# Optimization experiments

Hardware: AMD Instinct MI355X
Metric: run time of the kernel (lower is better)

The kernel has to match this reference:

```python
import jax, jax.numpy as jnp
import numpy as np

D_MODEL = 1024
NUM_HEADS = 16
D_K = D_MODEL // NUM_HEADS
THETA = 10000.0
BATCH, SEQ = 2, 2048


def setup_inputs() -> dict:
    key = jax.random.key(0)
    k1, k2, k3 = jax.random.split(key, 3)
    x = jax.random.normal(k1, (BATCH, SEQ, D_MODEL), dtype=jnp.float32)
    token_positions = jnp.arange(SEQ, dtype=jnp.int64 if jax.config.jax_enable_x64 else jnp.int32)
    # torch.nn.Linear convention: weight [out_features, in_features], y = x @ W.T
    w_qkv = jax.random.normal(k2, (3 * D_MODEL, D_MODEL), dtype=jnp.float32) * 0.02
    w_o = jax.random.normal(k3, (D_MODEL, D_MODEL), dtype=jnp.float32) * 0.02
    return {"x": x, "token_positions": token_positions, "w_qkv": w_qkv, "w_o": w_o}


def _rope(v, positions):
    # v: [B, H, S, d_k]; positions: [S] int
    half = D_K // 2
    inv_freq = THETA ** (-jnp.arange(0, half, dtype=jnp.float32) / half)  # [half]
    angles = positions.astype(jnp.float32)[:, None] * inv_freq[None, :]   # [S, half]
    cos = jnp.cos(angles)  # [S, half]
    sin = jnp.sin(angles)
    v1 = v[..., 0::2]  # even dims [B,H,S,half]
    v2 = v[..., 1::2]  # odd dims
    r1 = v1 * cos - v2 * sin
    r2 = v1 * sin + v2 * cos
    # interleave back to [..., d_k]
    return jnp.stack([r1, r2], axis=-1).reshape(v.shape)


def reference(x, token_positions, w_qkv, w_o):
    B, S, _ = x.shape
    # fused QKV projection: [B,S,3*D] -> [B,S,3,H,d_k]
    qkv = jnp.einsum("bsd,ed->bse", x, w_qkv).reshape(B, S, 3, NUM_HEADS, D_K)
    q = jnp.transpose(qkv[:, :, 0], (0, 2, 1, 3))
    k = jnp.transpose(qkv[:, :, 1], (0, 2, 1, 3))
    v = jnp.transpose(qkv[:, :, 2], (0, 2, 1, 3))
    q = _rope(q, token_positions)
    k = _rope(k, token_positions)
    scale = 1.0 / jnp.sqrt(jnp.float32(D_K))
    scores = jnp.einsum("bhqd,bhkd->bhqk", q, k) * scale  # [B,H,S,S]
    causal = jnp.tril(jnp.ones((S, S), dtype=bool))
    scores = jnp.where(causal, scores, jnp.float32(-jnp.inf))
    attn = jax.nn.softmax(scores, axis=-1)
    out = jnp.einsum("bhqk,bhkd->bhqd", attn, v)  # [B,H,S,d_k]
    out = jnp.transpose(out, (0, 2, 1, 3)).reshape(B, S, D_MODEL)
    return jnp.einsum("bsd,ed->bse", out, w_o)
```

## Files before the change

### kernel.cpp

```cpp
#include <hip/hip_runtime.h>
#include <cstdint>
#include <cstddef>
#include <cmath>

#define D_MODEL 1024
#define NHEADS  16
#define DK      64
#define SEQ     2048
#define NBATCH  2

#define NEG_BIG (-1e30f)

typedef __attribute__((ext_vector_type(8))) short bf16x8;
typedef __attribute__((ext_vector_type(4))) short bf16x4;
typedef __attribute__((ext_vector_type(4))) float f32x4;

#if defined(__AMDGCN__)
#define SETPRIO(p) __builtin_amdgcn_s_setprio(p)
#else
#define SETPRIO(p)
#endif

__device__ __forceinline__ float fexp2(float x) {
#if defined(__AMDGCN__) && __has_builtin(__builtin_amdgcn_exp2f)
  return __builtin_amdgcn_exp2f(x);
#else
  return exp2f(x);
#endif
}

__device__ inline f32x4 mfma16x16x16(bf16x4 a, bf16x4 b, f32x4 c) {
#if defined(__AMDGCN__)
# if __has_builtin(__builtin_amdgcn_mfma_f32_16x16x16_bf16)
  return __builtin_amdgcn_mfma_f32_16x16x16_bf16(a, b, c, 0, 0, 0);
# else
  return __builtin_amdgcn_mfma_f32_16x16x16bf16_1k(a, b, c, 0, 0, 0);
# endif
#else
  (void)a; (void)b;
  return c;
#endif
}

__device__ inline void gll16(const unsigned short* g, unsigned short* l) {
#if defined(__AMDGCN__)
  __builtin_amdgcn_global_load_lds(
      (const __attribute__((address_space(1))) void*)g,
      (__attribute__((address_space(3))) void*)l, 16, 0, 0);
#else
  (void)g; (void)l;
#endif
}

__device__ inline unsigned short f2bf(float f) {
  unsigned int u = __float_as_uint(f);
  u += 0x7fffu + ((u >> 16) & 1u);
  return (unsigned short)(u >> 16);
}

__device__ __forceinline__ unsigned cvtpk_bf16(float lo, float hi) {
#if defined(__AMDGCN__)
  unsigned r;
  asm("v_cvt_pk_bf16_f32 %0, %1, %2" : "=v"(r) : "v"(lo), "v"(hi));
  return r;
#else
  return (unsigned)f2bf(lo) | ((unsigned)f2bf(hi) << 16);
#endif
}

__device__ __forceinline__ void cvt_block(const void* src,
                                          unsigned short* dst, int i0) {
  const unsigned short* sp =
      (const unsigned short*)src + (size_t)i0 * 8 + threadIdx.x * 8;
  int cnt = 0;
#pragma unroll
  for (int j = 0; j < 8; j += 2) {
    const unsigned int u = sp[j];
    cnt += (((u >> 7) & 0xFFu) >= 0x84u) ? 1 : 0;
  }
  __shared__ int red[256];
  red[threadIdx.x] = cnt;
  __syncthreads();
  for (int s = 128; s > 0; s >>= 1) {
    if (threadIdx.x < s) red[threadIdx.x] += red[threadIdx.x + s];
    __syncthreads();
  }
  const bool isf32 = red[0] > 64;

  const int i = i0 + threadIdx.x;
  if (isf32) {
    const float4* s = (const float4*)src;
    float4 a = s[2 * i], b = s[2 * i + 1];
    uint4 r;
    r.x = (unsigned)f2bf(a.x) | ((unsigned)f2bf(a.y) << 16);
    r.y = (unsigned)f2bf(a.z) | ((unsigned)f2bf(a.w) << 16);
    r.z = (unsigned)f2bf(b.x) | ((unsigned)f2bf(b.y) << 16);
    r.w = (unsigned)f2bf(b.z) | ((unsigned)f2bf(b.w) << 16);
    ((uint4*)dst)[i] = r;
  } else {
    ((uint4*)dst)[i] = ((const uint4*)src)[i];
  }
}

__global__ __launch_bounds__(256) void cvt2_kernel(
    const void* __restrict__ srcA, unsigned short* __restrict__ dstA, int n8A,
    const void* __restrict__ srcB, unsigned short* __restrict__ dstB, int n8B) {
  const int bi = blockIdx.x;
  const int nblkA = n8A >> 8;
  (void)n8B;
  if (bi < nblkA) cvt_block(srcA, dstA, bi << 8);
  else            cvt_block(srcB, dstB, (bi - nblkA) << 8);
}

__global__ __launch_bounds__(256) void cvt3_kernel(
    const void* __restrict__ srcA, unsigned short* __restrict__ dstA, int n8A,
    const void* __restrict__ srcB, unsigned short* __restrict__ dstB, int n8B,
    const void* __restrict__ srcC, unsigned short* __restrict__ dstC) {
  const int bi = blockIdx.x;
  const int nblkA = n8A >> 8;
  const int nblkB = n8B >> 8;
  if (bi < nblkA)               cvt_block(srcA, dstA, bi << 8);
  else if (bi < nblkA + nblkB)  cvt_block(srcB, dstB, (bi - nblkA) << 8);
  else                          cvt_block(srcC, dstC, (bi - nblkA - nblkB) << 8);
}

template <int NF>
__device__ inline void gemm_bt_t(const unsigned short* __restrict__ A,
                                 const unsigned short* __restrict__ W,
                                 int m0, int n0,
                                 unsigned short* As, unsigned short* Bs,
                                 f32x4 (&acc)[NF][4]) {
  const int t    = threadIdx.x;
  const int lane = t & 63;
  const int w    = t >> 6;
  const int wm   = (w >> 1) * 64;
  const int wn   = (w & 1) * (NF * 16);
  const int frow = lane & 15;
  const int q4   = lane >> 4;

  for (int ft = 0; ft < NF; ++ft)
    for (int tt = 0; tt < 4; ++tt)
      acc[ft][tt] = (f32x4){0.f, 0.f, 0.f, 0.f};

  const int srow  = t >> 3;
  const int gslot = t & 7;

  for (int k0 = 0; k0 < 1024; k0 += 64) {
    __syncthreads();
#pragma unroll
    for (int c = 0; c < 4; ++c) {
      const int row = c * 32 + srow;
      const int gsrc = gslot ^ (row & 7);
      gll16(A + (size_t)(m0 + row) * 1024 + k0 + gsrc * 8,
            As + ((size_t)t + 256 * c) * 8);
    }
#pragma unroll
    for (int c = 0; c < NF; ++c) {
      const int row = c * 32 + srow;
      const int gsrc = gslot ^ (row & 7);
      gll16(W + (size_t)(n0 + row) * 1024 + k0 + gsrc * 8,
            Bs + ((size_t)t + 256 * c) * 8);
    }
    __syncthreads();

#pragma unroll
    for (int kk = 0; kk < 2; ++kk) {
      const int gg = q4 + kk * 4;
      bf16x8 xv[4], wv[NF];
#pragma unroll
      for (int tt = 0; tt < 4; ++tt) {
        const int row = wm + tt * 16 + frow;
        xv[tt] = *(const bf16x8*)(As + row * 64 + ((gg ^ (row & 7)) << 3));
      }
#pragma unroll
      for (int ft = 0; ft < NF; ++ft) {
        const int row = wn + ft * 16 + frow;
        wv[ft] = *(const bf16x8*)(Bs + row * 64 + ((gg ^ (row & 7)) << 3));
      }
#pragma unroll
      for (int ft = 0; ft < NF; ++ft)
#pragma unroll
        for (int tt = 0; tt < 4; ++tt)
          acc[ft][tt] = __builtin_amdgcn_mfma_f32_16x16x32_bf16(wv[ft], xv[tt],
                                                                acc[ft][tt], 0, 0, 0);
    }
  }
}

__global__ __launch_bounds__(256) void qkv_rope_kernel(
    const unsigned short* __restrict__ x,
    const unsigned short* __restrict__ wqkv,
    unsigned short* __restrict__ Qw, unsigned short* __restrict__ Kw,
    unsigned short* __restrict__ Vw) {
  __shared__ __align__(16) unsigned short As[128 * 64];
  __shared__ __align__(16) unsigned short Bs[128 * 64];
  f32x4 acc[4][4];
  const int lin = blockIdx.y * 32 + blockIdx.x;
  const int c8  = lin & 7;
  const int i   = lin >> 3;
  const int m0  = (c8 * 4 + (i & 3)) * 128;
  const int n0  = (i >> 2) * 128;
  gemm_bt_t<4>(x, wqkv, m0, n0, As, Bs, acc);

  const int t = threadIdx.x, lane = t & 63, w = t >> 6;
  const int wm = (w >> 1) * 64, wn = (w & 1) * 64;
  const int i16 = lane & 15, q4 = lane >> 4;
  const int part = n0 >> 10;
  const float LN_THETA_OVER_HALF = 0.2878231366242558f;
  const float SCALE_L2E = 0.18033688011112042f;

#pragma unroll
  for (int ft = 0; ft < 4; ++ft) {
    const int nb0 = n0 + wn + ft * 16 + (q4 << 2);
    const int h  = (nb0 >> 6) & 15;
    const int d0 = nb0 & 63;
    const float invf0 = __expf(-(float)(d0 >> 1) * LN_THETA_OVER_HALF);
    const float invf1 = __expf(-(float)((d0 >> 1) + 1) * LN_THETA_OVER_HALF);
#pragma unroll
    for (int tt = 0; tt < 4; ++tt) {
      const int m = m0 + wm + tt * 16 + i16;
      const int b = m >> 11, s = m & 2047;
      float v0 = acc[ft][tt][0], v1 = acc[ft][tt][1];
      float v2 = acc[ft][tt][2], v3 = acc[ft][tt][3];
      if (part < 2) {
        float sn0, cs0, sn1, cs1;
        __sincosf((float)s * invf0, &sn0, &cs0);
        __sincosf((float)s * invf1, &sn1, &cs1);
        const float r0 = v0 * cs0 - v1 * sn0;
        const float r1 = v0 * sn0 + v1 * cs0;
        const float r2 = v2 * cs1 - v3 * sn1;
        const float r3 = v2 * sn1 + v3 * cs1;
        v0 = r0; v1 = r1; v2 = r2; v3 = r3;
        if (part == 0) {
          v0 *= SCALE_L2E; v1 *= SCALE_L2E; v2 *= SCALE_L2E; v3 *= SCALE_L2E;
        }
        ushort4 pk;
        pk.x = f2bf(v0); pk.y = f2bf(v1); pk.z = f2bf(v2); pk.w = f2bf(v3);
        unsigned short* dst = (part == 0) ? Qw : Kw;
        *(ushort4*)(dst + (((size_t)(b * NHEADS + h)) * SEQ + s) * DK + d0) = pk;
      } else {
        unsigned short* vt =
            Vw + (((size_t)(b * NHEADS + h)) * DK + d0) * SEQ + s;
        vt[0]       = f2bf(v0);
        vt[SEQ]     = f2bf(v1);
        vt[2 * SEQ] = f2bf(v2);
        vt[3 * SEQ] = f2bf(v3);
      }
    }
  }
}

__device__ __forceinline__ void softmax_upd(
    const f32x4 (&s)[2][4], int q4,
    float& m_i, float& l_i, f32x4 o[4], bf16x4 (&pf)[2][4]) {
  float tm = NEG_BIG;
#pragma unroll
  for (int u = 0; u < 2; ++u)
#pragma unroll
    for (int mt = 0; mt < 4; ++mt)
#pragma unroll
      for (int r = 0; r < 4; ++r) tm = fmaxf(tm, s[u][mt][r]);
  tm = fmaxf(tm, __shfl_xor(tm, 16, 64));
  tm = fmaxf(tm, __shfl_xor(tm, 32, 64));
  const float m_new = fmaxf(m_i, tm);
  const float alpha = fexp2(m_i - m_new);
  m_i = m_new;

  float ls = 0.f;
#pragma unroll
  for (int u = 0; u < 2; ++u)
#pragma unroll
    for (int mt = 0; mt < 4; ++mt) {
      float p0 = fexp2(s[u][mt][0] - m_new);
      float p1 = fexp2(s[u][mt][1] - m_new);
      float p2 = fexp2(s[u][mt][2] - m_new);
      float p3 = fexp2(s[u][mt][3] - m_new);
      ls += (p0 + p1) + (p2 + p3);
      union { unsigned uu[2]; bf16x4 v; } pkk;
      pkk.uu[0] = cvtpk_bf16(p0, p1);
      pkk.uu[1] = cvtpk_bf16(p2, p3);
      pf[u][mt] = pkk.v;
    }
  ls += __shfl_xor(ls, 16, 64);
  ls += __shfl_xor(ls, 32, 64);
  l_i = l_i * alpha + ls;

  float a4[4];
#pragma unroll
  for (int r = 0; r < 4; ++r) a4[r] = __shfl(alpha, (q4 << 2) + r, 64);
#pragma unroll
  for (int n = 0; n < 4; ++n)
#pragma unroll
    for (int r = 0; r < 4; ++r) o[n][r] *= a4[r];
}

__device__ __forceinline__ void attn_step(
    const unsigned short* Ks0, const unsigned short* Ks1,
    const unsigned short* Vt0, const unsigned short* Vt1,
    bf16x8 qf0, bf16x8 qf1, int i16, int q4, int w,
    int q0t, int kt2, bool domask,
    float& m_i, float& l_i, f32x4 o_acc[4]) {
  f32x4 s_acc[2][4];
  SETPRIO(1);
#pragma unroll
  for (int u = 0; u < 2; ++u) {
    const unsigned short* Ksu = u ? Ks1 : Ks0;
#pragma unroll
    for (int mt = 0; mt < 4; ++mt) {
      const int key = mt * 16 + i16;
      const int k7 = key & 7;
      bf16x8 a0 = *(const bf16x8*)(Ksu + key * 64 + ((q4 ^ k7) << 3));
      bf16x8 a1 = *(const bf16x8*)(Ksu + key * 64 + (((4 + q4) ^ k7) << 3));
      f32x4 acc = (f32x4){0.f, 0.f, 0.f, 0.f};
      acc = __builtin_amdgcn_mfma_f32_16x16x32_bf16(a0, qf0, acc, 0, 0, 0);
      acc = __builtin_amdgcn_mfma_f32_16x16x32_bf16(a1, qf1, acc, 0, 0, 0);
      s_acc[u][mt] = acc;
    }
  }
  SETPRIO(0);

  if (domask) {
    const int qrow = q0t + w * 16 + i16;
#pragma unroll
    for (int u = 0; u < 2; ++u) {
      const int kb2 = (kt2 + u) * 64 + q4 * 4;
#pragma unroll
      for (int mt = 0; mt < 4; ++mt)
#pragma unroll
        for (int r = 0; r < 4; ++r)
          if (kb2 + mt * 16 + r > qrow) s_acc[u][mt][r] = NEG_BIG;
    }
  }

  bf16x4 pf[2][4];
  softmax_upd(s_acc, q4, m_i, l_i, o_acc, pf);

  SETPRIO(1);
#pragma unroll
  for (int u = 0; u < 2; ++u) {
    const unsigned short* Vtu = u ? Vt1 : Vt0;
#pragma unroll
    for (int mt = 0; mt < 4; ++mt) {
#pragma unroll
      for (int nt = 0; nt < 4; ++nt) {
        const int dk = nt * 16 + i16;
        const int slot = ((mt << 1) | (q4 >> 1)) ^ (dk & 7);
        bf16x4 vb = *(const bf16x4*)(Vtu + dk * 64 + (slot << 3) + ((q4 & 1) << 2));
        o_acc[nt] = mfma16x16x16(pf[u][mt], vb, o_acc[nt]);
      }
    }
  }
  SETPRIO(0);
}

__device__ __forceinline__ void attn_step2(
    const unsigned short* Ks0, const unsigned short* Ks1,
    const unsigned short* Vt0, const unsigned short* Vt1,
    bf16x8 qfB0, bf16x8 qfB1, bf16x8 qfA0, bf16x8 qfA1,
    int i16, int q4, int w, int q0A, int kt2, bool domaskA,
    float& mB, float& lB, f32x4 oB[4],
    float& mA, float& lA, f32x4 oA[4]) {
  f32x4 sB[2][4], sA[2][4];
  SETPRIO(1);
#pragma unroll
  for (int u = 0; u < 2; ++u) {
    const unsigned short* Ksu = u ? Ks1 : Ks0;
#pragma unroll
    for (int mt = 0; mt < 4; ++mt) {
      const int key = mt * 16 + i16;
      const int k7 = key & 7;
      bf16x8 a0 = *(const bf16x8*)(Ksu + key * 64 + ((q4 ^ k7) << 3));
      bf16x8 a1 = *(const bf16x8*)(Ksu + key * 64 + (((4 + q4) ^ k7) << 3));
      f32x4 ab = (f32x4){0.f, 0.f, 0.f, 0.f};
      ab = __builtin_amdgcn_mfma_f32_16x16x32_bf16(a0, qfB0, ab, 0, 0, 0);
      ab = __builtin_amdgcn_mfma_f32_16x16x32_bf16(a1, qfB1, ab, 0, 0, 0);
      sB[u][mt] = ab;
      f32x4 aa = (f32x4){0.f, 0.f, 0.f, 0.f};
      aa = __builtin_amdgcn_mfma_f32_16x16x32_bf16(a0, qfA0, aa, 0, 0, 0);
      aa = __builtin_amdgcn_mfma_f32_16x16x32_bf16(a1, qfA1, aa, 0, 0, 0);
      sA[u][mt] = aa;
    }
  }
  SETPRIO(0);

  if (domaskA) {
    const int qrow = q0A + w * 16 + i16;
#pragma unroll
    for (int u = 0; u < 2; ++u) {
      const int kb2 = (kt2 + u) * 64 + q4 * 4;
#pragma unroll
      for (int mt = 0; mt < 4; ++mt)
#pragma unroll
        for (int r = 0; r < 4; ++r)
          if (kb2 + mt * 16 + r > qrow) sA[u][mt][r] = NEG_BIG;
    }
  }

  bf16x4 pfB[2][4], pfA[2][4];
  softmax_upd(sB, q4, mB, lB, oB, pfB);
  softmax_upd(sA, q4, mA, lA, oA, pfA);

  SETPRIO(1);
#pragma unroll
  for (int u = 0; u < 2; ++u) {
    const unsigned short* Vtu = u ? Vt1 : Vt0;
#pragma unroll
    for (int mt = 0; mt < 4; ++mt) {
#pragma unroll
      for (int nt = 0; nt < 4; ++nt) {
        const int dk = nt * 16 + i16;
        const int slot = ((mt << 1) | (q4 >> 1)) ^ (dk & 7);
        bf16x4 vb = *(const bf16x4*)(Vtu + dk * 64 + (slot << 3) + ((q4 & 1) << 2));
        oB[nt] = mfma16x16x16(pfB[u][mt], vb, oB[nt]);
        oA[nt] = mfma16x16x16(pfA[u][mt], vb, oA[nt]);
      }
    }
  }
  SETPRIO(0);
}

__global__ __launch_bounds__(256, 2) void attn_mfma_kernel(
    const unsigned short* __restrict__ Q, const unsigned short* __restrict__ K,
    const unsigned short* __restrict__ VT, unsigned short* __restrict__ O) {
  __shared__ __align__(16) unsigned short Ks[2][2][64 * 64];
  __shared__ __align__(16) unsigned short Vt[2][2][64 * 64];

  const int t = threadIdx.x, w = t >> 6, lane = t & 63;
  const int i16 = lane & 15, q4 = lane >> 4;
  const int lin = blockIdx.y * 16 + blockIdx.x;
  const int c8  = lin & 7;
  const int j   = lin >> 3;
  const int bh  = c8 * 4 + (j & 3);
  const int qbA = j >> 2;
  const int qbB = 31 - qbA;
  const int q0A = qbA * 64, q0B = qbB * 64;
  const size_t base = (size_t)bh * SEQ * DK;

  const int srow  = t >> 3;
  const int gslot = t & 7;

  auto stage = [&](int p, int buf) {
#pragma unroll
    for (int c = 0; c < 4; ++c) {
      const int row = srow + 32 * c;
      const int gs  = gslot ^ (row & 7);
      gll16(K + base + (size_t)(p * 128 + row) * DK + gs * 8,
            &Ks[buf][0][0] + ((size_t)t + 256 * c) * 8);
    }
#pragma unroll
    for (int c = 0; c < 4; ++c) {
      const int row = srow + 32 * c;
      const int gs  = gslot ^ (row & 7);
      gll16(VT + base + (size_t)(row & 63) * SEQ
               + p * 128 + (row >> 6) * 64 + gs * 8,
            &Vt[buf][0][0] + ((size_t)t + 256 * c) * 8);
    }
  };

  bf16x8 qfA0, qfA1, qfB0, qfB1;
  {
    const unsigned short* qpA = Q + base + (size_t)(q0A + w * 16 + i16) * DK + q4 * 8;
    qfA0 = *(const bf16x8*)(qpA);
    qfA1 = *(const bf16x8*)(qpA + 32);
    const unsigned short* qpB = Q + base + (size_t)(q0B + w * 16 + i16) * DK + q4 * 8;
    qfB0 = *(const bf16x8*)(qpB);
    qfB1 = *(const bf16x8*)(qpB + 32);
  }

  f32x4 oA[4], oB[4];
#pragma unroll
  for (int n = 0; n < 4; ++n) {
    oA[n] = (f32x4){0.f, 0.f, 0.f, 0.f};
    oB[n] = (f32x4){0.f, 0.f, 0.f, 0.f};
  }
  float mA = NEG_BIG, lA = 0.f, mB = NEG_BIG, lB = 0.f;

  const int npairA = (qbA >> 1) + 1;
  const int npairB = (qbB >> 1) + 1;

  stage(0, 0);

  for (int pr = 0; pr < npairB; ++pr) {
    const int kt2 = pr * 2;
    const int cb = pr & 1;
    __syncthreads();
    if (pr + 1 < npairB) stage(pr + 1, cb ^ 1);

    if (pr < npairA) {
      attn_step2(Ks[cb][0], Ks[cb][1], Vt[cb][0], Vt[cb][1],
                 qfB0, qfB1, qfA0, qfA1, i16, q4, w,
                 q0A, kt2, pr == npairA - 1,
                 mB, lB, oB, mA, lA, oA);
    } else {
      attn_step(Ks[cb][0], Ks[cb][1], Vt[cb][0], Vt[cb][1], qfB0, qfB1,
                i16, q4, w, q0B, kt2, pr == npairB - 1, mB, lB, oB);
    }
  }

  const int b = bh >> 4, h = bh & 15;
#pragma unroll
  for (int r = 0; r < 4; ++r) {
    const float lrA = __shfl(lA, (q4 << 2) + r, 64);
    const float lrB = __shfl(lB, (q4 << 2) + r, 64);
    const float invA = 1.0f / lrA;
    const float invB = 1.0f / lrB;
    const int sA = q0A + w * 16 + (q4 << 2) + r;
    const int sB = q0B + w * 16 + (q4 << 2) + r;
#pragma unroll
    for (int nt = 0; nt < 4; ++nt) {
      const int dk = nt * 16 + i16;
      O[((size_t)(b * SEQ + sA)) * D_MODEL + h * DK + dk] = f2bf(oA[nt][r] * invA);
      O[((size_t)(b * SEQ + sB)) * D_MODEL + h * DK + dk] = f2bf(oB[nt][r] * invB);
    }
  }
}

__global__ __launch_bounds__(256) void oproj_kernel(
    const unsigned short* __restrict__ ain, const unsigned short* __restrict__ wo,
    float* __restrict__ out) {
  __shared__ __align__(16) unsigned short As[128 * 64];
  __shared__ __align__(16) unsigned short Bs[64 * 64];
  f32x4 acc[2][4];
  const int lin = blockIdx.y * 32 + blockIdx.x;
  const int c8  = lin & 7;
  const int i   = lin >> 3;
  const int m0  = (c8 * 4 + (i & 3)) * 128;
  const int n0  = (i >> 2) * 64;
  gemm_bt_t<2>(ain, wo, m0, n0, As, Bs, acc);

  const int t = threadIdx.x, lane = t & 63, w = t >> 6;
  const int wm = (w >> 1) * 64, wn = (w & 1) * 32;
  const int i16 = lane & 15, q4 = lane >> 4;
#pragma unroll
  for (int ft = 0; ft < 2; ++ft) {
    const int nb0 = n0 + wn + ft * 16 + (q4 << 2);
#pragma unroll
    for (int tt = 0; tt < 4; ++tt) {
      const int m = m0 + wm + tt * 16 + i16;
      float4 v;
      v.x = acc[ft][tt][0]; v.y = acc[ft][tt][1];
      v.z = acc[ft][tt][2]; v.w = acc[ft][tt][3];
      *(float4*)(out + (size_t)m * D_MODEL + nb0) = v;
    }
  }
}

extern "C" void kernel_launch(void* const* d_in, const int* in_sizes, int n_in,
                              void* d_out, int out_size, void* d_ws, size_t ws_size,
                              hipStream_t stream) {
  const void* x    = d_in[0];
  const void* wqkv = d_in[2];
  const void* wo   = d_in[3];
  float* out = (float*)d_out;

  const size_t NTOK  = (size_t)NBATCH * SEQ * D_MODEL;
  const size_t NWQKV = (size_t)3 * D_MODEL * D_MODEL;
  const size_t NWO   = (size_t)D_MODEL * D_MODEL;

  unsigned short* base = (unsigned short*)((char*)d_ws + 16);
  unsigned short* Qw = base;
  unsigned short* Kw = Qw + NTOK;
  unsigned short* Vw = Kw + NTOK;
  unsigned short* Aw = Vw + NTOK;
  unsigned short* xb = Aw;
  unsigned short* wq = Aw + NTOK;

  dim3 blk(256);

  const size_t need = 16 + (4 * NTOK + NWQKV + NWO) * sizeof(unsigned short);

  if (ws_size >= need) {
    unsigned short* wb = wq + NWQKV;
    hipLaunchKernelGGL(cvt3_kernel, dim3(4096), blk, 0, stream,
                       x, xb, (int)(NTOK / 8), wqkv, wq, (int)(NWQKV / 8),
                       wo, wb);

    dim3 g1(32, 24);
    hipLaunchKernelGGL(qkv_rope_kernel, g1, blk, 0, stream, xb, wq, Qw, Kw, Vw);

    dim3 g2(SEQ / 128, NBATCH * NHEADS);
    hipLaunchKernelGGL(attn_mfma_kernel, g2, blk, 0, stream, Qw, Kw, Vw, Aw);

    dim3 g3(32, 16);
    hipLaunchKernelGGL(oproj_kernel, g3, blk, 0, stream, Aw, wb, out);
  } else {
    unsigned short* wb = wq;
    hipLaunchKernelGGL(cvt2_kernel, dim3(3584), blk, 0, stream,
                       x, xb, (int)(NTOK / 8), wqkv, wq, (int)(NWQKV / 8));

    dim3 g1(32, 24);
    hipLaunchKernelGGL(qkv_rope_kernel, g1, blk, 0, stream, xb, wq, Qw, Kw, Vw);

    dim3 g2(SEQ / 128, NBATCH * NHEADS);
    hipLaunchKernelGGL(attn_mfma_kernel, g2, blk, 0, stream, Qw, Kw, Vw, Aw);

    hipLaunchKernelGGL(cvt2_kernel, dim3(512), blk, 0, stream,
                       wo, wb, (int)(NWO / 8), wo, wb, 0);

    dim3 g3(32, 16);
    hipLaunchKernelGGL(oproj_kernel, g3, blk, 0, stream, Aw, wb, out);
  }
}
```

Measured before the change: 182.8 us.

## Pair adjacent query blocks per workgroup and order longest pairs first

Each workgroup used to process query blocks qbA and 31-qbA, running a dual-Q step while both were active and a single-Q step afterwards. It now processes adjacent blocks 2p and 2p+1, which share the same key range, so every iteration is a dual-Q step with K/V reuse and the single-Q path is removed. Work per block is no longer balanced, so blocks are reordered to schedule the largest pairs first and reduce tail imbalance. In exchange, total work per block varies widely, and the final tile for block A computes a fully masked half.

After: 188.5 us. 1.03x slower.

```diff
diff --git a/kernel.cpp b/kernel.cpp
--- a/kernel.cpp
+++ b/kernel.cpp
@@ -294,70 +294,11 @@
     for (int r = 0; r < 4; ++r) o[n][r] *= a4[r];
 }
 
-__device__ __forceinline__ void attn_step(
-    const unsigned short* Ks0, const unsigned short* Ks1,
-    const unsigned short* Vt0, const unsigned short* Vt1,
-    bf16x8 qf0, bf16x8 qf1, int i16, int q4, int w,
-    int q0t, int kt2, bool domask,
-    float& m_i, float& l_i, f32x4 o_acc[4]) {
-  f32x4 s_acc[2][4];
-  SETPRIO(1);
-#pragma unroll
-  for (int u = 0; u < 2; ++u) {
-    const unsigned short* Ksu = u ? Ks1 : Ks0;
-#pragma unroll
-    for (int mt = 0; mt < 4; ++mt) {
-      const int key = mt * 16 + i16;
-      const int k7 = key & 7;
-      bf16x8 a0 = *(const bf16x8*)(Ksu + key * 64 + ((q4 ^ k7) << 3));
-      bf16x8 a1 = *(const bf16x8*)(Ksu + key * 64 + (((4 + q4) ^ k7) << 3));
-      f32x4 acc = (f32x4){0.f, 0.f, 0.f, 0.f};
-      acc = __builtin_amdgcn_mfma_f32_16x16x32_bf16(a0, qf0, acc, 0, 0, 0);
-      acc = __builtin_amdgcn_mfma_f32_16x16x32_bf16(a1, qf1, acc, 0, 0, 0);
-      s_acc[u][mt] = acc;
-    }
-  }
-  SETPRIO(0);
-
-  if (domask) {
-    const int qrow = q0t + w * 16 + i16;
-#pragma unroll
-    for (int u = 0; u < 2; ++u) {
-      const int kb2 = (kt2 + u) * 64 + q4 * 4;
-#pragma unroll
-      for (int mt = 0; mt < 4; ++mt)
-#pragma unroll
-        for (int r = 0; r < 4; ++r)
-          if (kb2 + mt * 16 + r > qrow) s_acc[u][mt][r] = NEG_BIG;
-    }
-  }
-
-  bf16x4 pf[2][4];
-  softmax_upd(s_acc, q4, m_i, l_i, o_acc, pf);
-
-  SETPRIO(1);
-#pragma unroll
-  for (int u = 0; u < 2; ++u) {
-    const unsigned short* Vtu = u ? Vt1 : Vt0;
-#pragma unroll
-    for (int mt = 0; mt < 4; ++mt) {
-#pragma unroll
-      for (int nt = 0; nt < 4; ++nt) {
-        const int dk = nt * 16 + i16;
-        const int slot = ((mt << 1) | (q4 >> 1)) ^ (dk & 7);
-        bf16x4 vb = *(const bf16x4*)(Vtu + dk * 64 + (slot << 3) + ((q4 & 1) << 2));
-        o_acc[nt] = mfma16x16x16(pf[u][mt], vb, o_acc[nt]);
-      }
-    }
-  }
-  SETPRIO(0);
-}
-
 __device__ __forceinline__ void attn_step2(
     const unsigned short* Ks0, const unsigned short* Ks1,
     const unsigned short* Vt0, const unsigned short* Vt1,
     bf16x8 qfB0, bf16x8 qfB1, bf16x8 qfA0, bf16x8 qfA1,
-    int i16, int q4, int w, int q0A, int kt2, bool domaskA,
+    int i16, int q4, int w, int q0A, int q0B, int kt2, bool domask,
     float& mB, float& lB, f32x4 oB[4],
     float& mA, float& lA, f32x4 oA[4]) {
   f32x4 sB[2][4], sA[2][4];
@@ -383,16 +324,20 @@
   }
   SETPRIO(0);
 
-  if (domaskA) {
-    const int qrow = q0A + w * 16 + i16;
+  if (domask) {
+    const int qrowA = q0A + w * 16 + i16;
+    const int qrowB = q0B + w * 16 + i16;
 #pragma unroll
     for (int u = 0; u < 2; ++u) {
       const int kb2 = (kt2 + u) * 64 + q4 * 4;
 #pragma unroll
       for (int mt = 0; mt < 4; ++mt)
 #pragma unroll
-        for (int r = 0; r < 4; ++r)
-          if (kb2 + mt * 16 + r > qrow) sA[u][mt][r] = NEG_BIG;
+        for (int r = 0; r < 4; ++r) {
+          const int kidx = kb2 + mt * 16 + r;
+          if (kidx > qrowA) sA[u][mt][r] = NEG_BIG;
+          if (kidx > qrowB) sB[u][mt][r] = NEG_BIG;
+        }
     }
   }
 
@@ -431,8 +376,10 @@
   const int c8  = lin & 7;
   const int j   = lin >> 3;
   const int bh  = c8 * 4 + (j & 3);
-  const int qbA = j >> 2;
-  const int qbB = 31 - qbA;
+  const int vv  = j >> 2;
+  const int pairIdx = (vv < 8) ? (15 - vv) : (vv - 8);
+  const int qbA = 2 * pairIdx;
+  const int qbB = qbA + 1;
   const int q0A = qbA * 64, q0B = qbB * 64;
   const size_t base = (size_t)bh * SEQ * DK;
 
@@ -475,26 +422,20 @@
   }
   float mA = NEG_BIG, lA = 0.f, mB = NEG_BIG, lB = 0.f;
 
-  const int npairA = (qbA >> 1) + 1;
-  const int npairB = (qbB >> 1) + 1;
+  const int npair = pairIdx + 1;
 
   stage(0, 0);
 
-  for (int pr = 0; pr < npairB; ++pr) {
+  for (int pr = 0; pr < npair; ++pr) {
     const int kt2 = pr * 2;
     const int cb = pr & 1;
     __syncthreads();
-    if (pr + 1 < npairB) stage(pr + 1, cb ^ 1);
-
-    if (pr < npairA) {
-      attn_step2(Ks[cb][0], Ks[cb][1], Vt[cb][0], Vt[cb][1],
-                 qfB0, qfB1, qfA0, qfA1, i16, q4, w,
-                 q0A, kt2, pr == npairA - 1,
-                 mB, lB, oB, mA, lA, oA);
-    } else {
-      attn_step(Ks[cb][0], Ks[cb][1], Vt[cb][0], Vt[cb][1], qfB0, qfB1,
-                i16, q4, w, q0B, kt2, pr == npairB - 1, mB, lB, oB);
-    }
+    if (pr + 1 < npair) stage(pr + 1, cb ^ 1);
+
+    attn_step2(Ks[cb][0], Ks[cb][1], Vt[cb][0], Vt[cb][1],
+               qfB0, qfB1, qfA0, qfA1, i16, q4, w,
+               q0A, q0B, kt2, pr == npair - 1,
+               mB, lB, oB, mA, lA, oA);
   }
 
   const int b = bh >> 4, h = bh & 15;
```
